# Kernel optimization log

Hardware: AMD Instinct MI355X
Metric: run time of the kernel (lower is better)

The kernel has to match this reference:

```python
import jax, jax.numpy as jnp
import numpy as np

D_MODEL = 1024
N_HEADS = 16
D_KEYS = D_MODEL // N_HEADS


def setup_inputs() -> dict:
    key = jax.random.key(0)
    ks = jax.random.split(key, 11)
    B, L, S = 2, 2048, 2048
    inp = {
        "queries": jax.random.normal(ks[0], (B, L, D_MODEL), dtype=jnp.float32),
        "keys": jax.random.normal(ks[1], (B, S, D_MODEL), dtype=jnp.float32),
        "values": jax.random.normal(ks[2], (B, S, D_MODEL), dtype=jnp.float32),
        # Linear params, scaled like torch default init (~U(-1/sqrt(D), 1/sqrt(D)))
        "Wq": jax.random.normal(ks[3], (D_MODEL, D_MODEL), dtype=jnp.float32) / np.sqrt(D_MODEL),
        "bq": jax.random.normal(ks[4], (D_MODEL,), dtype=jnp.float32) / np.sqrt(D_MODEL),
        "Wk": jax.random.normal(ks[5], (D_MODEL, D_MODEL), dtype=jnp.float32) / np.sqrt(D_MODEL),
        "bk": jax.random.normal(ks[6], (D_MODEL,), dtype=jnp.float32) / np.sqrt(D_MODEL),
        "Wv": jax.random.normal(ks[7], (D_MODEL, D_MODEL), dtype=jnp.float32) / np.sqrt(D_MODEL),
        "bv": jax.random.normal(ks[8], (D_MODEL,), dtype=jnp.float32) / np.sqrt(D_MODEL),
        "Wo": jax.random.normal(ks[9], (D_MODEL, D_MODEL), dtype=jnp.float32) / np.sqrt(D_MODEL),
        "bo": jax.random.normal(ks[10], (D_MODEL,), dtype=jnp.float32) / np.sqrt(D_MODEL),
    }
    return inp


def reference(queries, keys, values, Wq, bq, Wk, bk, Wv, bv, Wo, bo):
    B, L, _ = queries.shape
    S = keys.shape[1]
    H, E = N_HEADS, D_KEYS
    scale = E ** (-0.5)
    q = (queries @ Wq.T + bq).reshape(B, L, H, E)
    k = (keys @ Wk.T + bk).reshape(B, S, H, E)
    v = (values @ Wv.T + bv).reshape(B, S, H, E)
    scores = jnp.einsum('blhe,bshe->bhls', q, k)
    attn = jax.nn.softmax(scores * scale, axis=-1)  # dropout = identity in eval
    out = jnp.einsum('bhls,bshe->blhe', attn, v).reshape(B, L, H * E)
    return out @ Wo.T + bo
```

## Files before the change

kernel.cpp:

```cpp
#include <hip/hip_runtime.h>

typedef unsigned short u16;
typedef unsigned int u32;
typedef __attribute__((ext_vector_type(8))) short short8;
typedef __attribute__((ext_vector_type(4))) short s16x4;
typedef __attribute__((ext_vector_type(4))) float f32x4;
typedef __attribute__((ext_vector_type(16))) float f32x16;

#define DEVI __device__ __forceinline__

#define LSEQ 2048
#define DMODEL 1024
#define NH 16
#define EHD 64

#define QSCALE 0.18033688011112042f

#if __has_builtin(__builtin_amdgcn_exp2f)
#define EXP2(x) __builtin_amdgcn_exp2f(x)
#else
#define EXP2(x) exp2f(x)
#endif

DEVI u16 f2b(float f) {
    u32 u = __float_as_uint(f);
    return (u16)((u + 0x7FFFu + ((u >> 16) & 1u)) >> 16);
}

DEVI u32 cvtpk(float lo, float hi) {
    u32 r;
    asm("v_cvt_pk_bf16_f32 %0, %1, %2" : "=v"(r) : "v"(lo), "v"(hi));
    return r;
}

DEVI void swap32(u32& a, u32& b) {
    asm("v_permlane32_swap_b32 %0, %1" : "+v"(a), "+v"(b));
}

DEVI short8 mk8(u32 a0, u32 a1, u32 a2, u32 a3) {
    union { u32 u[4]; short8 s; } x;
    x.u[0] = a0; x.u[1] = a1; x.u[2] = a2; x.u[3] = a3;
    return x.s;
}

DEVI void async_cp16(const u16* g, u16* l) {
    __builtin_amdgcn_global_load_lds((const __attribute__((address_space(1))) u32*)g,
                                     (__attribute__((address_space(3))) u32*)l, 16, 0, 0);
}

DEVI short8 lds_swz(const u16* base, int row, int colb) {
    int off = (row << 7) + (colb ^ ((row & 7) << 4));
    return *(const short8*)((const char*)base + off);
}

__global__ __launch_bounds__(256) void cvt_all(const float* __restrict__ q,
                                               const float* __restrict__ k,
                                               const float* __restrict__ v,
                                               const float* __restrict__ wq,
                                               const float* __restrict__ wk,
                                               const float* __restrict__ wv,
                                               const float* __restrict__ wo,
                                               u16* __restrict__ dst) {
    const size_t NX8 = (size_t)2 * LSEQ * DMODEL / 8;
    const size_t NW8 = (size_t)DMODEL * DMODEL / 8;
    int bid = blockIdx.x;
    const float* src;
    size_t base;
    int rel;
    if (bid < 2048)      { src = q;  base = 0;             rel = bid; }
    else if (bid < 4096) { src = k;  base = NX8;           rel = bid - 2048; }
    else if (bid < 6144) { src = v;  base = 2 * NX8;       rel = bid - 4096; }
    else if (bid < 6656) { src = wq; base = 3 * NX8;             rel = bid - 6144; }
    else if (bid < 7168) { src = wk; base = 3 * NX8 + NW8;       rel = bid - 6656; }
    else if (bid < 7680) { src = wv; base = 3 * NX8 + 2 * NW8;   rel = bid - 7168; }
    else                 { src = wo; base = 3 * NX8 + 3 * NW8;   rel = bid - 7680; }
    size_t i = (size_t)rel * 256 + threadIdx.x;
    const float4* p = (const float4*)(src + i * 8);
    float4 a = p[0], c = p[1];
    short8 o;
    o[0] = (short)f2b(a.x); o[1] = (short)f2b(a.y);
    o[2] = (short)f2b(a.z); o[3] = (short)f2b(a.w);
    o[4] = (short)f2b(c.x); o[5] = (short)f2b(c.y);
    o[6] = (short)f2b(c.z); o[7] = (short)f2b(c.w);
    *(short8*)(dst + (base + i) * 8) = o;
}

__global__ __launch_bounds__(256) void gemm_qkv(const u16* __restrict__ X,
                                                const u16* __restrict__ W3,
                                                const float* __restrict__ bq,
                                                const float* __restrict__ bk,
                                                const float* __restrict__ bv,
                                                u16* __restrict__ Qp,
                                                u16* __restrict__ Kp,
                                                u16* __restrict__ Vt) {
    __shared__ __align__(16) u16 As[2][4096];
    __shared__ __align__(16) u16 Bs[2][4096];
    const int tid = threadIdx.x;
    const int lane = tid & 63, w = tid >> 6;
    const int lr = lane & 15, lk = lane >> 4;
    const int wr = w >> 1, wc = w & 1;
    const int rb = blockIdx.y * 128, cb = blockIdx.x * 128;
    const int K = DMODEL;
    const int seg = cb >> 10;
    const u16* A = X + (size_t)seg * ((size_t)2 * LSEQ * DMODEL);

    f32x4 acc[4][4] = {};

    const int arow = lane >> 2;
    const int acol = (lane & 3) * 8;

#define QKV_STAGE(bb, kk)                                                           \
    do {                                                                            \
        _Pragma("unroll") for (int c2 = 0; c2 < 2; ++c2) {                          \
            int c = w * 2 + c2;                                                     \
            async_cp16(A + (size_t)(rb + c * 16 + arow) * K + (kk) + acol,          \
                       &As[bb][c * 512]);                                           \
            async_cp16(W3 + (size_t)(cb + c * 16 + arow) * K + (kk) + acol,         \
                       &Bs[bb][c * 512]);                                           \
        }                                                                           \
    } while (0)

    QKV_STAGE(0, 0);
    asm volatile("s_waitcnt vmcnt(0)" ::: "memory");
    __syncthreads();

    int cur = 0;
    for (int k0 = 0; k0 < K; k0 += 32) {
        if (k0 + 32 < K) QKV_STAGE(cur ^ 1, k0 + 32);

        short8 af[4], bfr[4];
#pragma unroll
        for (int m = 0; m < 4; m++)
            af[m] = *(const short8*)(&As[cur][(wr * 64 + m * 16 + lr) * 32 + lk * 8]);
#pragma unroll
        for (int n = 0; n < 4; n++)
            bfr[n] = *(const short8*)(&Bs[cur][(wc * 64 + n * 16 + lr) * 32 + lk * 8]);
        __builtin_amdgcn_s_setprio(1);
#pragma unroll
        for (int m = 0; m < 4; m++)
#pragma unroll
            for (int n = 0; n < 4; n++)
                acc[m][n] = __builtin_amdgcn_mfma_f32_16x16x32_bf16(af[m], bfr[n], acc[m][n], 0, 0, 0);
        __builtin_amdgcn_s_setprio(0);

        asm volatile("s_waitcnt vmcnt(0)" ::: "memory");
        __syncthreads();
        cur ^= 1;
    }

    const float* bp = seg == 0 ? bq : (seg == 1 ? bk : bv);
    const float sc = seg == 0 ? QSCALE : 1.0f;

#pragma unroll
    for (int n = 0; n < 4; n++) {
        int col = cb + wc * 64 + n * 16 + lr;
        int c2 = col & 1023;
        float bvv = bp[c2];
#pragma unroll
        for (int m = 0; m < 4; m++) {
            int row0 = rb + wr * 64 + m * 16 + lk * 4;
            if (seg == 2) {
                s16x4 pk4;
#pragma unroll
                for (int r = 0; r < 4; r++) pk4[r] = (short)f2b(acc[m][n][r] + bvv);
                size_t idx = (((size_t)(row0 >> 11) * NH + (c2 >> 6)) * EHD + (c2 & 63)) * LSEQ +
                             (row0 & (LSEQ - 1));
                *(s16x4*)(Vt + idx) = pk4;
            } else {
                u16* dst = seg == 0 ? Qp : Kp;
#pragma unroll
                for (int r = 0; r < 4; r++)
                    dst[(size_t)(row0 + r) * DMODEL + c2] = f2b((acc[m][n][r] + bvv) * sc);
            }
        }
    }
}

__global__ __launch_bounds__(256) void gemm_out(const u16* __restrict__ A,
                                                const u16* __restrict__ B,
                                                const float* __restrict__ bias,
                                                float* __restrict__ C) {
    __shared__ __align__(16) u16 As[2][4096];
    __shared__ __align__(16) u16 Bs[2][2048];
    const int tid = threadIdx.x;
    const int lane = tid & 63, w = tid >> 6;
    const int lr = lane & 15, lk = lane >> 4;
    const int wr = w >> 1, wc = w & 1;
    const int rb = blockIdx.y * 128, cb = blockIdx.x * 64;
    const int K = DMODEL, N = DMODEL;

    f32x4 acc[4][2] = {};

    const int arow = lane >> 2;
    const int acol = (lane & 3) * 8;

#define OUT_STAGE(bb, kk)                                                           \
    do {                                                                            \
        _Pragma("unroll") for (int c2 = 0; c2 < 2; ++c2) {                          \
            int c = w * 2 + c2;                                                     \
            async_cp16(A + (size_t)(rb + c * 16 + arow) * K + (kk) + acol,          \
                       &As[bb][c * 512]);                                           \
        }                                                                           \
        async_cp16(B + (size_t)(cb + w * 16 + arow) * K + (kk) + acol,              \
                   &Bs[bb][w * 512]);                                               \
    } while (0)

    OUT_STAGE(0, 0);
    asm volatile("s_waitcnt vmcnt(0)" ::: "memory");
    __syncthreads();

    int cur = 0;
    for (int k0 = 0; k0 < K; k0 += 32) {
        if (k0 + 32 < K) OUT_STAGE(cur ^ 1, k0 + 32);

        short8 af[4], bfr[2];
#pragma unroll
        for (int m = 0; m < 4; m++)
            af[m] = *(const short8*)(&As[cur][(wr * 64 + m * 16 + lr) * 32 + lk * 8]);
#pragma unroll
        for (int n = 0; n < 2; n++)
            bfr[n] = *(const short8*)(&Bs[cur][(wc * 32 + n * 16 + lr) * 32 + lk * 8]);
        __builtin_amdgcn_s_setprio(1);
#pragma unroll
        for (int m = 0; m < 4; m++)
#pragma unroll
            for (int n = 0; n < 2; n++)
                acc[m][n] = __builtin_amdgcn_mfma_f32_16x16x32_bf16(af[m], bfr[n], acc[m][n], 0, 0, 0);
        __builtin_amdgcn_s_setprio(0);

        asm volatile("s_waitcnt vmcnt(0)" ::: "memory");
        __syncthreads();
        cur ^= 1;
    }

#pragma unroll
    for (int n = 0; n < 2; n++) {
        int col = cb + wc * 32 + n * 16 + lr;
        float bv = bias[col];
#pragma unroll
        for (int m = 0; m < 4; m++) {
            int row0 = rb + wr * 64 + m * 16 + lk * 4;
#pragma unroll
            for (int r = 0; r < 4; r++)
                C[(size_t)(row0 + r) * N + col] = acc[m][n][r] + bv;
        }
    }
}

__global__ __launch_bounds__(256) void attn_kernel(const u16* __restrict__ Q,
                                                   const u16* __restrict__ Kp,
                                                   const u16* __restrict__ Vtb,
                                                   u16* __restrict__ Hid) {
    const int bid = blockIdx.x;
    const int j = bid >> 3;
    const int bh = (bid & 7) + 8 * (j >> 4);
    const int q0 = (j & 15) * 128;
    const int b = bh >> 4, h = bh & 15;
    const int tid = threadIdx.x, lane = tid & 63, w = tid >> 6;
    const int l31 = lane & 31, hi = lane >> 5;
    const int qb = q0 + w * 32;

    __shared__ __align__(16) u16 Ks[2][4096];
    __shared__ __align__(16) u16 Vs[2][4096];

    short8 qf[4];
#pragma unroll
    for (int eg = 0; eg < 4; eg++)
        qf[eg] = *(const short8*)(Q + (size_t)(b * LSEQ + qb + l31) * DMODEL + h * EHD +
                                  eg * 16 + hi * 8);

    const int colb = (((lane & 7) ^ (lane >> 3)) << 4);
    size_t kbase[2], vbase[2];
#pragma unroll
    for (int jj = 0; jj < 2; jj++) {
        int row = (jj * 4 + w) * 8 + (lane >> 3);
        kbase[jj] = (size_t)(b * LSEQ + row) * DMODEL + h * EHD + (colb >> 1);
        vbase[jj] = ((size_t)bh * EHD + row) * LSEQ + (colb >> 1);
    }

#define ATTN_STAGE(bb, s0v)                                                           \
    do {                                                                              \
        async_cp16(Kp + kbase[0] + (size_t)(s0v)*DMODEL, &Ks[bb][(0 * 4 + w) * 512]); \
        async_cp16(Kp + kbase[1] + (size_t)(s0v)*DMODEL, &Ks[bb][(1 * 4 + w) * 512]); \
        async_cp16(Vtb + vbase[0] + (s0v), &Vs[bb][(0 * 4 + w) * 512]);               \
        async_cp16(Vtb + vbase[1] + (s0v), &Vs[bb][(1 * 4 + w) * 512]);               \
    } while (0)

    f32x16 o0 = (f32x16)0.f, o1 = (f32x16)0.f, lsum = (f32x16)0.f;
    const u32 one2 = 0x3F803F80u;
    const short8 ones = mk8(one2, one2, one2, one2);

    ATTN_STAGE(0, 0);
    asm volatile("s_waitcnt vmcnt(0)" ::: "memory");
    __syncthreads();

    int cur = 0;
    for (int t = 0; t < LSEQ / 64; ++t) {
        if (t + 1 < LSEQ / 64) ATTN_STAGE(cur ^ 1, (t + 1) * 64);

        f32x16 s0 = (f32x16)0.f, s1 = (f32x16)0.f;
        __builtin_amdgcn_s_setprio(1);
#pragma unroll
        for (int eg = 0; eg < 4; eg++) {
            short8 kf0 = lds_swz(&Ks[cur][0], l31, eg * 32 + hi * 16);
            short8 kf1 = lds_swz(&Ks[cur][0], 32 + l31, eg * 32 + hi * 16);
            s0 = __builtin_amdgcn_mfma_f32_32x32x16_bf16(kf0, qf[eg], s0, 0, 0, 0);
            s1 = __builtin_amdgcn_mfma_f32_32x32x16_bf16(kf1, qf[eg], s1, 0, 0, 0);
        }
        __builtin_amdgcn_s_setprio(0);

#pragma unroll
        for (int r = 0; r < 16; r++) {
            s0[r] = EXP2(s0[r]);
            s1[r] = EXP2(s1[r]);
        }

        short8 paf[4];
#pragma unroll
        for (int kc = 0; kc < 4; kc++) {
            int ro = (kc & 1) * 8;
            u32 u0, u1, u2, u3;
            if (kc < 2) {
                u0 = cvtpk(s0[ro + 0], s0[ro + 1]); u1 = cvtpk(s0[ro + 2], s0[ro + 3]);
                u2 = cvtpk(s0[ro + 4], s0[ro + 5]); u3 = cvtpk(s0[ro + 6], s0[ro + 7]);
            } else {
                u0 = cvtpk(s1[ro + 0], s1[ro + 1]); u1 = cvtpk(s1[ro + 2], s1[ro + 3]);
                u2 = cvtpk(s1[ro + 4], s1[ro + 5]); u3 = cvtpk(s1[ro + 6], s1[ro + 7]);
            }
            swap32(u0, u2);
            swap32(u1, u3);
            paf[kc] = mk8(u0, u1, u2, u3);
        }

        __builtin_amdgcn_s_setprio(1);
#pragma unroll
        for (int kc = 0; kc < 4; kc++) {
            short8 vf0 = lds_swz(&Vs[cur][0], l31, kc * 32 + hi * 16);
            short8 vf1 = lds_swz(&Vs[cur][0], 32 + l31, kc * 32 + hi * 16);
            o0 = __builtin_amdgcn_mfma_f32_32x32x16_bf16(paf[kc], vf0, o0, 0, 0, 0);
            o1 = __builtin_amdgcn_mfma_f32_32x32x16_bf16(paf[kc], vf1, o1, 0, 0, 0);
            lsum = __builtin_amdgcn_mfma_f32_32x32x16_bf16(paf[kc], ones, lsum, 0, 0, 0);
        }
        __builtin_amdgcn_s_setprio(0);

        asm volatile("s_waitcnt vmcnt(0)" ::: "memory");
        __syncthreads();
        cur ^= 1;
    }

#pragma unroll
    for (int r = 0; r < 16; r++) {
        float li = 1.0f / lsum[r];
        int qrow = qb + (r & 3) + 8 * (r >> 2) + 4 * hi;
        size_t base = (size_t)(b * LSEQ + qrow) * DMODEL + h * EHD;
        Hid[base + l31] = f2b(o0[r] * li);
        Hid[base + 32 + l31] = f2b(o1[r] * li);
    }
}

extern "C" void kernel_launch(void* const* d_in, const int* in_sizes, int n_in,
                              void* d_out, int out_size, void* d_ws, size_t ws_size,
                              hipStream_t stream) {
    const float* queries = (const float*)d_in[0];
    const float* keys    = (const float*)d_in[1];
    const float* values  = (const float*)d_in[2];
    const float* Wq = (const float*)d_in[3];
    const float* bq = (const float*)d_in[4];
    const float* Wk = (const float*)d_in[5];
    const float* bk = (const float*)d_in[6];
    const float* Wv = (const float*)d_in[7];
    const float* bv = (const float*)d_in[8];
    const float* Wo = (const float*)d_in[9];
    const float* bo = (const float*)d_in[10];
    float* out = (float*)d_out;

    const size_t NX = (size_t)2 * LSEQ * DMODEL;
    const size_t NW = (size_t)DMODEL * DMODEL;

    u16* p = (u16*)d_ws;
    u16* Xq = p;  p += NX;
    u16* Xk = p;  p += NX;
    u16* Xv = p;  p += NX;
    u16* Wqb = p; p += NW;
    u16* Wkb = p; p += NW;
    u16* Wvb = p; p += NW;
    u16* Wob = p; p += NW;
    u16* Qp = p;  p += NX;
    u16* Kp = p;  p += NX;
    u16* Vt = p;  p += NX;
    u16* Hid = p; p += NX;
    (void)Xk; (void)Xv; (void)Wkb; (void)Wvb;

    cvt_all<<<8192, 256, 0, stream>>>(queries, keys, values, Wq, Wk, Wv, Wo, Xq);

    gemm_qkv<<<dim3(3 * DMODEL / 128, (2 * LSEQ) / 128), 256, 0, stream>>>(
        Xq, Wqb, bq, bk, bv, Qp, Kp, Vt);

    attn_kernel<<<512, 256, 0, stream>>>(Qp, Kp, Vt, Hid);

    gemm_out<<<dim3(DMODEL / 64, (2 * LSEQ) / 128), 256, 0, stream>>>(Hid, Wob, bo, out);
}
```

Measured before the change: 139.9 us.

## Triple-buffer GEMM K-loop and remap blocks for XCD-local row reuse

```diff
diff --git a/kernel.cpp b/kernel.cpp
--- a/kernel.cpp
+++ b/kernel.cpp
@@ -93,15 +93,19 @@
                                                 u16* __restrict__ Qp,
                                                 u16* __restrict__ Kp,
                                                 u16* __restrict__ Vt) {
-    __shared__ __align__(16) u16 As[2][4096];
-    __shared__ __align__(16) u16 Bs[2][4096];
+    __shared__ __align__(16) u16 As[3][4096];
+    __shared__ __align__(16) u16 Bs[3][4096];
     const int tid = threadIdx.x;
     const int lane = tid & 63, w = tid >> 6;
     const int lr = lane & 15, lk = lane >> 4;
     const int wr = w >> 1, wc = w & 1;
-    const int rb = blockIdx.y * 128, cb = blockIdx.x * 128;
+    const int bid = blockIdx.x;
+    const int xcd = bid & 7, rr = bid >> 3;
+    const int rb = (xcd * 4 + rr / 24) * 128;
+    const int xtile = rr % 24;
+    const int cb = xtile * 128;
     const int K = DMODEL;
-    const int seg = cb >> 10;
+    const int seg = xtile >> 3;
     const u16* A = X + (size_t)seg * ((size_t)2 * LSEQ * DMODEL);
 
     f32x4 acc[4][4] = {};
@@ -120,33 +124,37 @@
         }                                                                           \
     } while (0)
 
+#define QKV_ITER(bc, bs, tt)                                                          \
+    do {                                                                              \
+        if ((tt) + 2 < 32) QKV_STAGE(bs, ((tt) + 2) * 32);                            \
+        short8 af[4], bfr[4];                                                         \
+        _Pragma("unroll") for (int m = 0; m < 4; m++)                                 \
+            af[m] = *(const short8*)(&As[bc][(wr * 64 + m * 16 + lr) * 32 + lk * 8]); \
+        _Pragma("unroll") for (int n = 0; n < 4; n++)                                 \
+            bfr[n] = *(const short8*)(&Bs[bc][(wc * 64 + n * 16 + lr) * 32 + lk * 8]); \
+        __builtin_amdgcn_s_setprio(1);                                                \
+        _Pragma("unroll") for (int m = 0; m < 4; m++)                                 \
+            _Pragma("unroll") for (int n = 0; n < 4; n++)                             \
+                acc[m][n] =                                                           \
+                    __builtin_amdgcn_mfma_f32_16x16x32_bf16(af[m], bfr[n], acc[m][n], 0, 0, 0); \
+        __builtin_amdgcn_s_setprio(0);                                                \
+        if ((tt) + 2 < 32) asm volatile("s_waitcnt vmcnt(4)" ::: "memory");           \
+        else               asm volatile("s_waitcnt vmcnt(0)" ::: "memory");           \
+        __builtin_amdgcn_s_barrier();                                                 \
+    } while (0)
+
     QKV_STAGE(0, 0);
-    asm volatile("s_waitcnt vmcnt(0)" ::: "memory");
-    __syncthreads();
-
-    int cur = 0;
-    for (int k0 = 0; k0 < K; k0 += 32) {
-        if (k0 + 32 < K) QKV_STAGE(cur ^ 1, k0 + 32);
-
-        short8 af[4], bfr[4];
-#pragma unroll
-        for (int m = 0; m < 4; m++)
-            af[m] = *(const short8*)(&As[cur][(wr * 64 + m * 16 + lr) * 32 + lk * 8]);
-#pragma unroll
-        for (int n = 0; n < 4; n++)
-            bfr[n] = *(const short8*)(&Bs[cur][(wc * 64 + n * 16 + lr) * 32 + lk * 8]);
-        __builtin_amdgcn_s_setprio(1);
-#pragma unroll
-        for (int m = 0; m < 4; m++)
-#pragma unroll
-            for (int n = 0; n < 4; n++)
-                acc[m][n] = __builtin_amdgcn_mfma_f32_16x16x32_bf16(af[m], bfr[n], acc[m][n], 0, 0, 0);
-        __builtin_amdgcn_s_setprio(0);
-
-        asm volatile("s_waitcnt vmcnt(0)" ::: "memory");
-        __syncthreads();
-        cur ^= 1;
-    }
+    QKV_STAGE(1, 32);
+    asm volatile("s_waitcnt vmcnt(4)" ::: "memory");
+    __builtin_amdgcn_s_barrier();
+
+    for (int tb = 0; tb < 30; tb += 3) {
+        QKV_ITER(0, 2, tb);
+        QKV_ITER(1, 0, tb + 1);
+        QKV_ITER(2, 1, tb + 2);
+    }
+    QKV_ITER(0, 2, 30);
+    QKV_ITER(1, 0, 31);
 
     const float* bp = seg == 0 ? bq : (seg == 1 ? bk : bv);
     const float sc = seg == 0 ? QSCALE : 1.0f;
@@ -180,13 +188,16 @@
                                                 const u16* __restrict__ B,
                                                 const float* __restrict__ bias,
                                                 float* __restrict__ C) {
-    __shared__ __align__(16) u16 As[2][4096];
-    __shared__ __align__(16) u16 Bs[2][2048];
+    __shared__ __align__(16) u16 As[3][4096];
+    __shared__ __align__(16) u16 Bs[3][2048];
     const int tid = threadIdx.x;
     const int lane = tid & 63, w = tid >> 6;
     const int lr = lane & 15, lk = lane >> 4;
     const int wr = w >> 1, wc = w & 1;
-    const int rb = blockIdx.y * 128, cb = blockIdx.x * 64;
+    const int bid = blockIdx.x;
+    const int xcd = bid & 7, rr = bid >> 3;
+    const int rb = (xcd * 4 + rr / 16) * 128;
+    const int cb = (rr % 16) * 64;
     const int K = DMODEL, N = DMODEL;
 
     f32x4 acc[4][2] = {};
@@ -205,33 +216,37 @@
                    &Bs[bb][w * 512]);                                               \
     } while (0)
 
+#define OUT_ITER(bc, bs, tt)                                                          \
+    do {                                                                              \
+        if ((tt) + 2 < 32) OUT_STAGE(bs, ((tt) + 2) * 32);                            \
+        short8 af[4], bfr[2];                                                         \
+        _Pragma("unroll") for (int m = 0; m < 4; m++)                                 \
+            af[m] = *(const short8*)(&As[bc][(wr * 64 + m * 16 + lr) * 32 + lk * 8]); \
+        _Pragma("unroll") for (int n = 0; n < 2; n++)                                 \
+            bfr[n] = *(const short8*)(&Bs[bc][(wc * 32 + n * 16 + lr) * 32 + lk * 8]); \
+        __builtin_amdgcn_s_setprio(1);                                                \
+        _Pragma("unroll") for (int m = 0; m < 4; m++)                                 \
+            _Pragma("unroll") for (int n = 0; n < 2; n++)                             \
+                acc[m][n] =                                                           \
+                    __builtin_amdgcn_mfma_f32_16x16x32_bf16(af[m], bfr[n], acc[m][n], 0, 0, 0); \
+        __builtin_amdgcn_s_setprio(0);                                                \
+        if ((tt) + 2 < 32) asm volatile("s_waitcnt vmcnt(3)" ::: "memory");           \
+        else               asm volatile("s_waitcnt vmcnt(0)" ::: "memory");           \
+        __builtin_amdgcn_s_barrier();                                                 \
+    } while (0)
+
     OUT_STAGE(0, 0);
-    asm volatile("s_waitcnt vmcnt(0)" ::: "memory");
-    __syncthreads();
-
-    int cur = 0;
-    for (int k0 = 0; k0 < K; k0 += 32) {
-        if (k0 + 32 < K) OUT_STAGE(cur ^ 1, k0 + 32);
-
-        short8 af[4], bfr[2];
-#pragma unroll
-        for (int m = 0; m < 4; m++)
-            af[m] = *(const short8*)(&As[cur][(wr * 64 + m * 16 + lr) * 32 + lk * 8]);
-#pragma unroll
-        for (int n = 0; n < 2; n++)
-            bfr[n] = *(const short8*)(&Bs[cur][(wc * 32 + n * 16 + lr) * 32 + lk * 8]);
-        __builtin_amdgcn_s_setprio(1);
-#pragma unroll
-        for (int m = 0; m < 4; m++)
-#pragma unroll
-            for (int n = 0; n < 2; n++)
-                acc[m][n] = __builtin_amdgcn_mfma_f32_16x16x32_bf16(af[m], bfr[n], acc[m][n], 0, 0, 0);
-        __builtin_amdgcn_s_setprio(0);
-
-        asm volatile("s_waitcnt vmcnt(0)" ::: "memory");
-        __syncthreads();
-        cur ^= 1;
-    }
+    OUT_STAGE(1, 32);
+    asm volatile("s_waitcnt vmcnt(3)" ::: "memory");
+    __builtin_amdgcn_s_barrier();
+
+    for (int tb = 0; tb < 30; tb += 3) {
+        OUT_ITER(0, 2, tb);
+        OUT_ITER(1, 0, tb + 1);
+        OUT_ITER(2, 1, tb + 2);
+    }
+    OUT_ITER(0, 2, 30);
+    OUT_ITER(1, 0, 31);
 
 #pragma unroll
     for (int n = 0; n < 2; n++) {
@@ -393,10 +408,9 @@
 
     cvt_all<<<8192, 256, 0, stream>>>(queries, keys, values, Wq, Wk, Wv, Wo, Xq);
 
-    gemm_qkv<<<dim3(3 * DMODEL / 128, (2 * LSEQ) / 128), 256, 0, stream>>>(
-        Xq, Wqb, bq, bk, bv, Qp, Kp, Vt);
+    gemm_qkv<<<768, 256, 0, stream>>>(Xq, Wqb, bq, bk, bv, Qp, Kp, Vt);
 
     attn_kernel<<<512, 256, 0, stream>>>(Qp, Kp, Vt, Hid);
 
-    gemm_out<<<dim3(DMODEL / 64, (2 * LSEQ) / 128), 256, 0, stream>>>(Hid, Wob, bo, out);
-}
+    gemm_out<<<512, 256, 0, stream>>>(Hid, Wob, bo, out);
+}
```

New measurement: 136.7 us. 1.02x faster.
